# Kernel tuning notes

Measured on AMD Instinct MI355X. Metric: run time of the kernel, lower is better.

Reference implementation:

```python
import jax, jax.numpy as jnp
import numpy as np

NUM_CLASSES = 33  # labels 0..32; class 0 = background, 32 instances
EPS = 1e-06


def _lovasz_hinge_flat(logits, labels):
    # logits, labels: flat 1-D float arrays (labels in {0,1})
    signs = 2.0 * labels - 1.0
    errors = 1.0 - logits * signs
    order = jnp.argsort(-errors)            # descending sort
    errors_sorted = errors[order]
    gt_sorted = labels[order]
    gts = jnp.sum(gt_sorted)
    intersection = gts - jnp.cumsum(gt_sorted)
    union = gts + jnp.cumsum(1.0 - gt_sorted)
    jaccard = 1.0 - intersection / union
    grad = jnp.concatenate([jaccard[:1], jaccard[1:] - jaccard[:-1]])
    return jnp.dot(jax.nn.relu(errors_sorted), grad)


def _per_sample_loss(y_emb, y_sig, gt_patch):
    # y_emb: [2,H,W] float, y_sig: [1,H,W] float, gt_patch: [1,H,W] int
    # to_onehot(gt)[0, 1:] -> [N,H,W], N = NUM_CLASSES-1 instance channels
    gt_one_hot = jax.nn.one_hot(gt_patch[0], NUM_CLASSES, axis=0, dtype=y_emb.dtype)[1:]
    counts = jnp.sum(gt_one_hot, axis=(1, 2), keepdims=True)          # [N,1,1]
    # per-instance embedding centers: [2,N,1,1]
    centers = jnp.sum(gt_one_hot[None] * y_emb[:, None], axis=(2, 3), keepdims=True) / counts
    instance_sigmas = gt_one_hot[None] * y_sig[:, None]               # [1,N,H,W]
    sigmas = jnp.sum(instance_sigmas, axis=(2, 3), keepdims=True) / counts  # [1,N,1,1]
    var_sigmas = jnp.sum(((instance_sigmas - jax.lax.stop_gradient(sigmas)) * gt_one_hot) ** 2) / counts  # [N,1,1]
    center_dist = jnp.linalg.norm(centers - y_emb[:, None], axis=0)   # [N,H,W]
    probs = jnp.exp(-0.5 * (center_dist / sigmas) ** 2)               # [1,N,H,W]
    logits = (probs * 2.0 - 1.0).reshape(-1)
    labels = jnp.broadcast_to(gt_one_hot[None], probs.shape).reshape(-1)
    return _lovasz_hinge_flat(logits, labels) + jnp.mean(var_sigmas)


def setup_inputs() -> dict:
    key = jax.random.key(0)
    k1, k2, k3 = jax.random.split(key, 3)
    B, H, W = 4, 512, 512
    y_embeddings = jax.random.normal(k1, (B, 2, H, W), dtype=jnp.float32)
    y_sigma = jax.random.uniform(k2, (B, 1, H, W), dtype=jnp.float32)
    y_true = jax.random.randint(k3, (B, 1, H, W), 0, NUM_CLASSES, dtype=jnp.int64)
    return {"y_embeddings": y_embeddings, "y_sigma": y_sigma, "y_true": y_true}


def reference(y_embeddings, y_sigma, y_true):
    # Assumes every sample contains foreground (random labels over 512x512
    # guarantee this w.h.p.), so the torch `if torch.any(gt>0)` branch is taken
    # for all samples and the final loss is the mean over the batch.
    losses = jax.vmap(_per_sample_loss)(y_embeddings, y_sigma, y_true)
    return jnp.mean(losses)
```

## Files before the change

### kernel.cpp

```cpp
#include <hip/hip_runtime.h>

#define HW    262144
#define BNUM  4
#define NC    33
#define NI    32

#define NB     2048
#define TMAX   16.0f
#define BSCALE 128.0f
#define EG     8192
#define ESCALE 4096.0f

typedef unsigned long long ull;

#define W_TH   0
#define W_E0   4096
#define W_E1   (W_E0 + NC)
#define W_SS   (W_E1 + NC)
#define W_SS2  (W_SS + NC)
#define W_CNT  (W_SS2 + NC)
#define W_LOSS (W_CNT + NC)
#define W_STRIDE 4272

__global__ void __launch_bounds__(256) stats_kernel(
    const float* __restrict__ emb, const float* __restrict__ sig,
    const int* __restrict__ gt, float* __restrict__ ws) {
  int s = blockIdx.y;
  float* wsS = ws + (size_t)s * W_STRIDE;
  __shared__ float a0[4][NC], a1[4][NC], as_[4][NC], as2[4][NC];
  __shared__ unsigned ac[4][NC];
  int t = threadIdx.x;
  int w = t >> 6;
  for (int k = t; k < 4 * NC; k += 256) {
    ((float*)a0)[k] = 0.f; ((float*)a1)[k] = 0.f;
    ((float*)as_)[k] = 0.f; ((float*)as2)[k] = 0.f;
    ((unsigned*)ac)[k] = 0u;
  }
  __syncthreads();
  const float* e0p = emb + (size_t)s * 2 * HW;
  const float* e1p = e0p + HW;
  const float* sp  = sig + (size_t)s * HW;
  const int*   gp  = gt  + (size_t)s * HW;
  int base = blockIdx.x * 1024;
  #pragma unroll
  for (int i = 0; i < 2; ++i) {
    int idx = base + i * 512 + t * 2;
    int2  lb = *(const int2*)(gp + idx);
    float2 x = *(const float2*)(e0p + idx);
    float2 y = *(const float2*)(e1p + idx);
    float2 sg = *(const float2*)(sp + idx);
    if (lb.x > 0) {
      atomicAdd(&a0[w][lb.x], x.x); atomicAdd(&a1[w][lb.x], y.x);
      atomicAdd(&as_[w][lb.x], sg.x); atomicAdd(&as2[w][lb.x], sg.x * sg.x);
      atomicAdd(&ac[w][lb.x], 1u);
    }
    if (lb.y > 0) {
      atomicAdd(&a0[w][lb.y], x.y); atomicAdd(&a1[w][lb.y], y.y);
      atomicAdd(&as_[w][lb.y], sg.y); atomicAdd(&as2[w][lb.y], sg.y * sg.y);
      atomicAdd(&ac[w][lb.y], 1u);
    }
  }
  __syncthreads();
  if (t >= 1 && t < NC) {
    float s0 = a0[0][t] + a0[1][t] + a0[2][t] + a0[3][t];
    float s1 = a1[0][t] + a1[1][t] + a1[2][t] + a1[3][t];
    float ss = as_[0][t] + as_[1][t] + as_[2][t] + as_[3][t];
    float s2 = as2[0][t] + as2[1][t] + as2[2][t] + as2[3][t];
    unsigned c = ac[0][t] + ac[1][t] + ac[2][t] + ac[3][t];
    if (c) {
      atomicAdd(&wsS[W_E0 + t], s0);
      atomicAdd(&wsS[W_E1 + t], s1);
      atomicAdd(&wsS[W_SS + t], ss);
      atomicAdd(&wsS[W_SS2 + t], s2);
      atomicAdd((unsigned*)wsS + (W_CNT + t), c);
    }
  }
}

__global__ void __launch_bounds__(512) hist_kernel(
    const float* __restrict__ emb, const int* __restrict__ gt,
    float* __restrict__ ws) {
  int s = blockIdx.y;
  float* wsS = ws + (size_t)s * W_STRIDE;
  __shared__ unsigned hist[NB * 4];
  __shared__ float c0s[NC], c1s[NC], qs[NC];
  int t = threadIdx.x;
  int r = t & 3;
  for (int k = t; k < NB * 4; k += 512) hist[k] = 0u;
  if (t >= 1 && t < NC) {
    float inv = 1.0f / (float)((const unsigned*)wsS)[W_CNT + t];
    c0s[t] = wsS[W_E0 + t] * inv;
    c1s[t] = wsS[W_E1 + t] * inv;
    float sg = wsS[W_SS + t] * inv;
    qs[t] = 0.5f / (sg * sg);
  }
  __syncthreads();
  const float* e0p = emb + (size_t)s * 2 * HW;
  const float* e1p = e0p + HW;
  const int*   gp  = gt  + (size_t)s * HW;
  int idx = blockIdx.x * 1024 + t * 2;
  int2   lb = *(const int2*)(gp + idx);
  float2 px = *(const float2*)(e0p + idx);
  float2 py = *(const float2*)(e1p + idx);
  #pragma unroll 4
  for (int n = 1; n <= NI; ++n) {
    float c0 = c0s[n], c1 = c1s[n], q = qs[n];
    {
      float dx = c0 - px.x, dy = c1 - py.x;
      float tt = (dx * dx + dy * dy) * q;
      bool pos = (lb.x == n);
      if (pos || tt < TMAX) {
        int b = (int)(tt * BSCALE); if (b > NB - 1) b = NB - 1;
        atomicAdd(&hist[(b << 2) | r], pos ? 0x10000u : 1u);
      }
    }
    {
      float dx = c0 - px.y, dy = c1 - py.y;
      float tt = (dx * dx + dy * dy) * q;
      bool pos = (lb.y == n);
      if (pos || tt < TMAX) {
        int b = (int)(tt * BSCALE); if (b > NB - 1) b = NB - 1;
        atomicAdd(&hist[(b << 2) | r], pos ? 0x10000u : 1u);
      }
    }
  }
  __syncthreads();
  ull* th = (ull*)wsS;
  for (int k = t; k < NB; k += 512) {
    unsigned v = hist[k * 4] + hist[k * 4 + 1] + hist[k * 4 + 2] + hist[k * 4 + 3];
    if (v) {
      ull add = ((ull)(v >> 16) << 32) | (v & 0xFFFFu);
      atomicAdd(&th[k], add);
    }
  }
}

__global__ void __launch_bounds__(512) scan_kernel(float* __restrict__ ws) {
  int s = blockIdx.x;
  float* wsS = ws + (size_t)s * W_STRIDE;
  const ull* th = (const ull*)wsS;
  const unsigned* wsu = (const unsigned*)wsS;
  __shared__ unsigned ep[EG], en[EG];
  __shared__ ull wsum[8];
  __shared__ float red[8];
  __shared__ float vart_s;
  int t = threadIdx.x;
  int lane = t & 63, wid = t >> 6;
  for (int k = t; k < EG; k += 512) { ep[k] = 0u; en[k] = 0u; }
  if (wid == 0) {
    float S = 0.f, rc = 0.f;
    if (lane >= 1 && lane < NC) {
      float c = (float)wsu[W_CNT + lane];
      float sg = wsS[W_SS + lane] / c;
      S = wsS[W_SS2 + lane] - c * sg * sg;
      rc = 1.0f / c;
    }
    for (int o = 32; o; o >>= 1) {
      S  += __shfl_down(S, o);
      rc += __shfl_down(rc, o);
    }
    if (lane == 0) vart_s = S * rc / (float)NI;
  }
  __syncthreads();
  for (int b = t; b < NB; b += 512) {
    ull v = th[b];
    unsigned pos = (unsigned)(v >> 32), neg = (unsigned)(v & 0xFFFFFFFFu);
    if (pos | neg) {
      float tc = ((float)b + 0.5f) * (1.0f / BSCALE);
      float ex = __expf(-tc);
      if (pos) {
        float e = 2.0f - 2.0f * ex;
        int k = (int)(e * ESCALE); if (k > EG - 1) k = EG - 1;
        atomicAdd(&ep[k], pos);
      }
      if (neg) {
        float e = 2.0f * ex;
        int k = (int)(e * ESCALE); if (k > EG - 1) k = EG - 1;
        atomicAdd(&en[k], neg);
      }
    }
  }
  __syncthreads();
  const int CH = EG / 512;
  int j0 = t * CH;
  unsigned np = 0, nn = 0;
  for (int k = 0; k < CH; ++k) {
    int b = EG - 1 - (j0 + k);
    np += ep[b]; nn += en[b];
  }
  ull v = ((ull)np << 32) | (ull)nn;
  ull inc = v;
  for (int o = 1; o < 64; o <<= 1) {
    ull u = __shfl_up(inc, o);
    if (lane >= o) inc += u;
  }
  if (lane == 63) wsum[wid] = inc;
  __syncthreads();
  ull offset = 0, total = 0;
  for (int i = 0; i < 8; ++i) {
    ull x = wsum[i];
    if (i < wid) offset += x;
    total += x;
  }
  ull excl = offset + inc - v;
  float P = (float)(unsigned)(total >> 32);
  unsigned p = (unsigned)(excl >> 32), f = (unsigned)(excl & 0xFFFFFFFFu);
  float jprev = 1.0f - (P - (float)p) / (P + (float)f);
  float contrib = 0.f;
  for (int k = 0; k < CH; ++k) {
    int b = EG - 1 - (j0 + k);
    unsigned ap_ = ep[b], an_ = en[b];
    if (ap_ | an_) {
      p += ap_; f += an_;
      float j = 1.0f - (P - (float)p) / (P + (float)f);
      float e = ((float)b + 0.5f) * (2.0f / EG);
      contrib += e * (j - jprev);
      jprev = j;
    }
  }
  for (int o = 32; o; o >>= 1) contrib += __shfl_down(contrib, o);
  if (lane == 0) red[wid] = contrib;
  __syncthreads();
  if (t == 0) {
    float tot = 0.f;
    for (int i = 0; i < 8; ++i) tot += red[i];
    wsS[W_LOSS] = tot + vart_s;
  }
}

__global__ void final_kernel(const float* __restrict__ ws, float* __restrict__ out) {
  float a = 0.f;
  for (int s = 0; s < BNUM; ++s) a += ws[(size_t)s * W_STRIDE + W_LOSS];
  out[0] = 0.25f * a;
}

extern "C" void kernel_launch(void* const* d_in, const int* in_sizes, int n_in,
                              void* d_out, int out_size, void* d_ws, size_t ws_size,
                              hipStream_t stream) {
  const float* emb = (const float*)d_in[0];
  const float* sig = (const float*)d_in[1];
  const int*   gt  = (const int*)d_in[2];
  float* out = (float*)d_out;
  float* ws  = (float*)d_ws;

  hipMemsetAsync(d_ws, 0, (size_t)BNUM * W_STRIDE * sizeof(float), stream);

  dim3 gA(256, BNUM);
  stats_kernel<<<gA, 256, 0, stream>>>(emb, sig, gt, ws);
  dim3 gB(256, BNUM);
  hist_kernel<<<gB, 512, 0, stream>>>(emb, gt, ws);
  scan_kernel<<<BNUM, 512, 0, stream>>>(ws);
  final_kernel<<<1, 1, 0, stream>>>(ws, out);
}
```

Baseline: 133.9 us.

## Vectorize loads, expand distance algebraically, and fuse scan with final reduction

The stats and hist kernels now load float4/int4 instead of float2/int2. The hist grid is halved so each thread handles four pixels. The squared distance is expanded into a precomputed quadratic form (Q·|p|² + linear terms + constant) with the bin scale folded in, which removes the per-instance subtraction and the separate TMAX test. The per-sample scan and the final mean are merged into one single-block kernel that loops over samples, saving a launch but serializing the four scans onto one CU. The expanded form may lose float precision through cancellation near the centers.

```diff
diff --git a/kernel.cpp b/kernel.cpp
--- a/kernel.cpp
+++ b/kernel.cpp
@@ -6,7 +6,6 @@
 #define NI    32
 
 #define NB     2048
-#define TMAX   16.0f
 #define BSCALE 128.0f
 #define EG     8192
 #define ESCALE 4096.0f
@@ -41,25 +40,22 @@
   const float* e1p = e0p + HW;
   const float* sp  = sig + (size_t)s * HW;
   const int*   gp  = gt  + (size_t)s * HW;
-  int base = blockIdx.x * 1024;
-  #pragma unroll
-  for (int i = 0; i < 2; ++i) {
-    int idx = base + i * 512 + t * 2;
-    int2  lb = *(const int2*)(gp + idx);
-    float2 x = *(const float2*)(e0p + idx);
-    float2 y = *(const float2*)(e1p + idx);
-    float2 sg = *(const float2*)(sp + idx);
-    if (lb.x > 0) {
-      atomicAdd(&a0[w][lb.x], x.x); atomicAdd(&a1[w][lb.x], y.x);
-      atomicAdd(&as_[w][lb.x], sg.x); atomicAdd(&as2[w][lb.x], sg.x * sg.x);
-      atomicAdd(&ac[w][lb.x], 1u);
-    }
-    if (lb.y > 0) {
-      atomicAdd(&a0[w][lb.y], x.y); atomicAdd(&a1[w][lb.y], y.y);
-      atomicAdd(&as_[w][lb.y], sg.y); atomicAdd(&as2[w][lb.y], sg.y * sg.y);
-      atomicAdd(&ac[w][lb.y], 1u);
-    }
-  }
+  int idx = blockIdx.x * 1024 + t * 4;
+  int4   lb = *(const int4*)(gp + idx);
+  float4 x  = *(const float4*)(e0p + idx);
+  float4 y  = *(const float4*)(e1p + idx);
+  float4 sg = *(const float4*)(sp + idx);
+#define ACC(L, X, Y, SG)                                              \
+  if (L > 0) {                                                        \
+    atomicAdd(&a0[w][L], X); atomicAdd(&a1[w][L], Y);                 \
+    atomicAdd(&as_[w][L], SG); atomicAdd(&as2[w][L], (SG) * (SG));    \
+    atomicAdd(&ac[w][L], 1u);                                         \
+  }
+  ACC(lb.x, x.x, y.x, sg.x)
+  ACC(lb.y, x.y, y.y, sg.y)
+  ACC(lb.z, x.z, y.z, sg.z)
+  ACC(lb.w, x.w, y.w, sg.w)
+#undef ACC
   __syncthreads();
   if (t >= 1 && t < NC) {
     float s0 = a0[0][t] + a0[1][t] + a0[2][t] + a0[3][t];
@@ -83,46 +79,53 @@
   int s = blockIdx.y;
   float* wsS = ws + (size_t)s * W_STRIDE;
   __shared__ unsigned hist[NB * 4];
-  __shared__ float c0s[NC], c1s[NC], qs[NC];
+  __shared__ float4 cons[NC];
   int t = threadIdx.x;
   int r = t & 3;
   for (int k = t; k < NB * 4; k += 512) hist[k] = 0u;
   if (t >= 1 && t < NC) {
     float inv = 1.0f / (float)((const unsigned*)wsS)[W_CNT + t];
-    c0s[t] = wsS[W_E0 + t] * inv;
-    c1s[t] = wsS[W_E1 + t] * inv;
-    float sg = wsS[W_SS + t] * inv;
-    qs[t] = 0.5f / (sg * sg);
+    float c0 = wsS[W_E0 + t] * inv;
+    float c1 = wsS[W_E1 + t] * inv;
+    float sgm = wsS[W_SS + t] * inv;
+    float Q = 0.5f / (sgm * sgm) * BSCALE;
+    float4 c;
+    c.x = Q;
+    c.y = -2.0f * Q * c0;
+    c.z = -2.0f * Q * c1;
+    c.w = Q * (c0 * c0 + c1 * c1);
+    cons[t] = c;
   }
   __syncthreads();
   const float* e0p = emb + (size_t)s * 2 * HW;
   const float* e1p = e0p + HW;
   const int*   gp  = gt  + (size_t)s * HW;
-  int idx = blockIdx.x * 1024 + t * 2;
-  int2   lb = *(const int2*)(gp + idx);
-  float2 px = *(const float2*)(e0p + idx);
-  float2 py = *(const float2*)(e1p + idx);
+  int idx = blockIdx.x * 2048 + t * 4;
+  int4   lb = *(const int4*)(gp + idx);
+  float4 px = *(const float4*)(e0p + idx);
+  float4 py = *(const float4*)(e1p + idx);
+  float4 ss;
+  ss.x = fmaf(px.x, px.x, py.x * py.x);
+  ss.y = fmaf(px.y, px.y, py.y * py.y);
+  ss.z = fmaf(px.z, px.z, py.z * py.z);
+  ss.w = fmaf(px.w, px.w, py.w * py.w);
+  unsigned* hr = hist + r;
   #pragma unroll 4
   for (int n = 1; n <= NI; ++n) {
-    float c0 = c0s[n], c1 = c1s[n], q = qs[n];
-    {
-      float dx = c0 - px.x, dy = c1 - py.x;
-      float tt = (dx * dx + dy * dy) * q;
-      bool pos = (lb.x == n);
-      if (pos || tt < TMAX) {
-        int b = (int)(tt * BSCALE); if (b > NB - 1) b = NB - 1;
-        atomicAdd(&hist[(b << 2) | r], pos ? 0x10000u : 1u);
-      }
-    }
-    {
-      float dx = c0 - px.y, dy = c1 - py.y;
-      float tt = (dx * dx + dy * dy) * q;
-      bool pos = (lb.y == n);
-      if (pos || tt < TMAX) {
-        int b = (int)(tt * BSCALE); if (b > NB - 1) b = NB - 1;
-        atomicAdd(&hist[(b << 2) | r], pos ? 0x10000u : 1u);
-      }
-    }
+    float4 C = cons[n];
+#define ITEM(P0, P1, SV, L)                                            \
+    {                                                                  \
+      float bf = fmaf(C.x, SV, fmaf(C.y, P0, fmaf(C.z, P1, C.w)));     \
+      int ib = (int)bf;                                                \
+      bool pos = (L == n);                                             \
+      if (pos) ib = min(ib, NB - 1);                                   \
+      if (ib < NB) atomicAdd(&hr[ib << 2], pos ? 0x10000u : 1u);       \
+    }
+    ITEM(px.x, py.x, ss.x, lb.x)
+    ITEM(px.y, py.y, ss.y, lb.y)
+    ITEM(px.z, py.z, ss.z, lb.z)
+    ITEM(px.w, py.w, ss.w, lb.w)
+#undef ITEM
   }
   __syncthreads();
   ull* th = (ull*)wsS;
@@ -135,103 +138,102 @@
   }
 }
 
-__global__ void __launch_bounds__(512) scan_kernel(float* __restrict__ ws) {
-  int s = blockIdx.x;
-  float* wsS = ws + (size_t)s * W_STRIDE;
-  const ull* th = (const ull*)wsS;
-  const unsigned* wsu = (const unsigned*)wsS;
+__global__ void __launch_bounds__(512) scan_final_kernel(
+    float* __restrict__ ws, float* __restrict__ out) {
   __shared__ unsigned ep[EG], en[EG];
   __shared__ ull wsum[8];
   __shared__ float red[8];
   __shared__ float vart_s;
   int t = threadIdx.x;
   int lane = t & 63, wid = t >> 6;
-  for (int k = t; k < EG; k += 512) { ep[k] = 0u; en[k] = 0u; }
-  if (wid == 0) {
-    float S = 0.f, rc = 0.f;
-    if (lane >= 1 && lane < NC) {
-      float c = (float)wsu[W_CNT + lane];
-      float sg = wsS[W_SS + lane] / c;
-      S = wsS[W_SS2 + lane] - c * sg * sg;
-      rc = 1.0f / c;
-    }
-    for (int o = 32; o; o >>= 1) {
-      S  += __shfl_down(S, o);
-      rc += __shfl_down(rc, o);
-    }
-    if (lane == 0) vart_s = S * rc / (float)NI;
-  }
-  __syncthreads();
-  for (int b = t; b < NB; b += 512) {
-    ull v = th[b];
-    unsigned pos = (unsigned)(v >> 32), neg = (unsigned)(v & 0xFFFFFFFFu);
-    if (pos | neg) {
-      float tc = ((float)b + 0.5f) * (1.0f / BSCALE);
-      float ex = __expf(-tc);
-      if (pos) {
-        float e = 2.0f - 2.0f * ex;
-        int k = (int)(e * ESCALE); if (k > EG - 1) k = EG - 1;
-        atomicAdd(&ep[k], pos);
-      }
-      if (neg) {
-        float e = 2.0f * ex;
-        int k = (int)(e * ESCALE); if (k > EG - 1) k = EG - 1;
-        atomicAdd(&en[k], neg);
-      }
-    }
-  }
-  __syncthreads();
-  const int CH = EG / 512;
-  int j0 = t * CH;
-  unsigned np = 0, nn = 0;
-  for (int k = 0; k < CH; ++k) {
-    int b = EG - 1 - (j0 + k);
-    np += ep[b]; nn += en[b];
-  }
-  ull v = ((ull)np << 32) | (ull)nn;
-  ull inc = v;
-  for (int o = 1; o < 64; o <<= 1) {
-    ull u = __shfl_up(inc, o);
-    if (lane >= o) inc += u;
-  }
-  if (lane == 63) wsum[wid] = inc;
-  __syncthreads();
-  ull offset = 0, total = 0;
-  for (int i = 0; i < 8; ++i) {
-    ull x = wsum[i];
-    if (i < wid) offset += x;
-    total += x;
-  }
-  ull excl = offset + inc - v;
-  float P = (float)(unsigned)(total >> 32);
-  unsigned p = (unsigned)(excl >> 32), f = (unsigned)(excl & 0xFFFFFFFFu);
-  float jprev = 1.0f - (P - (float)p) / (P + (float)f);
-  float contrib = 0.f;
-  for (int k = 0; k < CH; ++k) {
-    int b = EG - 1 - (j0 + k);
-    unsigned ap_ = ep[b], an_ = en[b];
-    if (ap_ | an_) {
-      p += ap_; f += an_;
-      float j = 1.0f - (P - (float)p) / (P + (float)f);
-      float e = ((float)b + 0.5f) * (2.0f / EG);
-      contrib += e * (j - jprev);
-      jprev = j;
-    }
-  }
-  for (int o = 32; o; o >>= 1) contrib += __shfl_down(contrib, o);
-  if (lane == 0) red[wid] = contrib;
-  __syncthreads();
-  if (t == 0) {
-    float tot = 0.f;
-    for (int i = 0; i < 8; ++i) tot += red[i];
-    wsS[W_LOSS] = tot + vart_s;
-  }
-}
-
-__global__ void final_kernel(const float* __restrict__ ws, float* __restrict__ out) {
-  float a = 0.f;
-  for (int s = 0; s < BNUM; ++s) a += ws[(size_t)s * W_STRIDE + W_LOSS];
-  out[0] = 0.25f * a;
+  float acc = 0.f;
+  for (int s = 0; s < BNUM; ++s) {
+    float* wsS = ws + (size_t)s * W_STRIDE;
+    const ull* th = (const ull*)wsS;
+    const unsigned* wsu = (const unsigned*)wsS;
+    for (int k = t; k < EG; k += 512) { ep[k] = 0u; en[k] = 0u; }
+    if (wid == 0) {
+      float S = 0.f, rc = 0.f;
+      if (lane >= 1 && lane < NC) {
+        float c = (float)wsu[W_CNT + lane];
+        float sg = wsS[W_SS + lane] / c;
+        S = wsS[W_SS2 + lane] - c * sg * sg;
+        rc = 1.0f / c;
+      }
+      for (int o = 32; o; o >>= 1) {
+        S  += __shfl_down(S, o);
+        rc += __shfl_down(rc, o);
+      }
+      if (lane == 0) vart_s = S * rc / (float)NI;
+    }
+    __syncthreads();
+    for (int b = t; b < NB; b += 512) {
+      ull v = th[b];
+      unsigned pos = (unsigned)(v >> 32), neg = (unsigned)(v & 0xFFFFFFFFu);
+      if (pos | neg) {
+        float tc = ((float)b + 0.5f) * (1.0f / BSCALE);
+        float ex = __expf(-tc);
+        if (pos) {
+          float e = 2.0f - 2.0f * ex;
+          int k = (int)(e * ESCALE); if (k > EG - 1) k = EG - 1;
+          atomicAdd(&ep[k], pos);
+        }
+        if (neg) {
+          float e = 2.0f * ex;
+          int k = (int)(e * ESCALE); if (k > EG - 1) k = EG - 1;
+          atomicAdd(&en[k], neg);
+        }
+      }
+    }
+    __syncthreads();
+    const int CH = EG / 512;
+    int j0 = t * CH;
+    unsigned np = 0, nn = 0;
+    for (int k = 0; k < CH; ++k) {
+      int b = EG - 1 - (j0 + k);
+      np += ep[b]; nn += en[b];
+    }
+    ull v = ((ull)np << 32) | (ull)nn;
+    ull inc = v;
+    for (int o = 1; o < 64; o <<= 1) {
+      ull u = __shfl_up(inc, o);
+      if (lane >= o) inc += u;
+    }
+    if (lane == 63) wsum[wid] = inc;
+    __syncthreads();
+    ull offset = 0, total = 0;
+    for (int i = 0; i < 8; ++i) {
+      ull x = wsum[i];
+      if (i < wid) offset += x;
+      total += x;
+    }
+    ull excl = offset + inc - v;
+    float P = (float)(unsigned)(total >> 32);
+    unsigned p = (unsigned)(excl >> 32), f = (unsigned)(excl & 0xFFFFFFFFu);
+    float jprev = 1.0f - (P - (float)p) / (P + (float)f);
+    float contrib = 0.f;
+    for (int k = 0; k < CH; ++k) {
+      int b = EG - 1 - (j0 + k);
+      unsigned ap_ = ep[b], an_ = en[b];
+      if (ap_ | an_) {
+        p += ap_; f += an_;
+        float j = 1.0f - (P - (float)p) / (P + (float)f);
+        float e = ((float)b + 0.5f) * (2.0f / EG);
+        contrib += e * (j - jprev);
+        jprev = j;
+      }
+    }
+    for (int o = 32; o; o >>= 1) contrib += __shfl_down(contrib, o);
+    if (lane == 0) red[wid] = contrib;
+    __syncthreads();
+    if (t == 0) {
+      float tot = 0.f;
+      for (int i = 0; i < 8; ++i) tot += red[i];
+      acc += tot + vart_s;
+    }
+    __syncthreads();
+  }
+  if (t == 0) out[0] = acc * (1.0f / BNUM);
 }
 
 extern "C" void kernel_launch(void* const* d_in, const int* in_sizes, int n_in,
@@ -247,8 +249,7 @@
 
   dim3 gA(256, BNUM);
   stats_kernel<<<gA, 256, 0, stream>>>(emb, sig, gt, ws);
-  dim3 gB(256, BNUM);
+  dim3 gB(128, BNUM);
   hist_kernel<<<gB, 512, 0, stream>>>(emb, gt, ws);
-  scan_kernel<<<BNUM, 512, 0, stream>>>(ws);
-  final_kernel<<<1, 1, 0, stream>>>(ws, out);
-}
+  scan_final_kernel<<<1, 512, 0, stream>>>(ws, out);
+}
```

Result: slower. 149.3 us (+11.5%).
